# Optimization experiments

Hardware: AMD Instinct MI355X
Metric: run time of the kernel (lower is better)

The kernel has to match this reference:

```python
import jax, jax.numpy as jnp
import numpy as np

N_R, N_S, D, L = 20000, 5000, 512, 3

def setup_inputs() -> dict:
    key = jax.random.key(0)
    ks = jax.random.split(key, 7)
    s = 1.0 / np.sqrt(D)  # xavier-ish scale to keep activations bounded
    return {
        "h_s": jax.random.normal(ks[0], (N_S, D), jnp.float32),
        "A_rs": jax.random.uniform(ks[1], (N_R, N_S), jnp.float32),
        "r_embed": jax.random.normal(ks[2], (N_R, D), jnp.float32) * s,
        "Wr": jax.random.normal(ks[3], (L, D, D), jnp.float32) * s,  # reading self-transform per layer
        "Ws": jax.random.normal(ks[4], (L, D, D), jnp.float32) * s,  # skill->reading cross-transform
        "Vr": jax.random.normal(ks[5], (L, D, D), jnp.float32) * s,  # reading->skill cross-transform
        "Vs": jax.random.normal(ks[6], (L, D, D), jnp.float32) * s,  # skill self-transform
    }

def reference(h_s, A_rs, r_embed, Wr, Ws, Vr, Vs):
    # ReadingGCNStage.forward: h = dropout(r_embed.weight) (eval-mode no-op),
    # then BipartiteGCNStack(h_s, h, A_rs): per-layer degree-normalized bipartite
    # message passing with dense per-side transforms and ReLU.
    eps = 1e-6
    deg_r = A_rs.sum(axis=1, keepdims=True) + eps   # [N_R, 1] reading degrees
    deg_s = A_rs.sum(axis=0)[:, None] + eps          # [N_S, 1] skill degrees
    h_r = r_embed
    for l in range(Wr.shape[0]):  # fixed small n_layers
        m_r = (A_rs @ h_s) / deg_r        # [N_R, D] mean-aggregated skill msgs
        m_s = (A_rs.T @ h_r) / deg_s      # [N_S, D] mean-aggregated reading msgs
        h_r_new = jax.nn.relu(m_r @ Ws[l] + h_r @ Wr[l])
        h_s = jax.nn.relu(m_s @ Vr[l] + h_s @ Vs[l])
        h_r = h_r_new
    return h_r  # updated reading embeddings [N_R, D]
```

## Files before the change

### kernel.cpp

```cpp
#include <hip/hip_runtime.h>


typedef __bf16 bf16_t;
typedef __attribute__((ext_vector_type(8))) __bf16 bf16x8;
typedef __attribute__((ext_vector_type(4))) __bf16 bf16x4;
typedef __attribute__((ext_vector_type(4))) float f32x4;

#define N_R 20000
#define N_S 5000
#define DD  512
#define MR_PAD 20096
#define MS_PAD 5120
#define KS_PAD 5056
#define KR_PAD 20224

__device__ __forceinline__ void gll16(const bf16_t* g, bf16_t* l) {
  __builtin_amdgcn_global_load_lds(
      (const __attribute__((address_space(1))) void*)g,
      (__attribute__((address_space(3))) void*)l, 16, 0, 0);
}


__global__ __launch_bounds__(256) void conv_rowsum_A(
    const float* __restrict__ A, bf16_t* __restrict__ Ab, float* __restrict__ deg_r) {
  int r = blockIdx.x;
  int t = threadIdx.x;
  __shared__ float wsum[4];
  if (r < N_R) {
    const float4* Arow = (const float4*)(A + (size_t)r * N_S);
    float s = 0.f;
    for (int c4 = t; c4 < N_S / 4; c4 += 256) {
      float4 v = Arow[c4];
      s += v.x + v.y + v.z + v.w;
      bf16x4 pv;
      pv[0] = (bf16_t)v.x; pv[1] = (bf16_t)v.y; pv[2] = (bf16_t)v.z; pv[3] = (bf16_t)v.w;
      *(bf16x4*)(Ab + (size_t)r * KS_PAD + 4 * c4) = pv;
    }
    if (t < KS_PAD - N_S) Ab[(size_t)r * KS_PAD + N_S + t] = (bf16_t)0.f;
    for (int off = 32; off > 0; off >>= 1) s += __shfl_down(s, off, 64);
    if ((t & 63) == 0) wsum[t >> 6] = s;
    __syncthreads();
    if (t == 0) deg_r[r] = wsum[0] + wsum[1] + wsum[2] + wsum[3] + 1e-6f;
  } else {
    for (int c = t; c < KS_PAD; c += 256) Ab[(size_t)r * KS_PAD + c] = (bf16_t)0.f;
  }
}

__global__ void init_deg_s(float* __restrict__ deg_s) {
  int i = blockIdx.x * 256 + threadIdx.x;
  if (i < N_S) deg_s[i] = 1e-6f;
}

__global__ __launch_bounds__(256) void transpose_A_deg(
    const bf16_t* __restrict__ Ab, bf16_t* __restrict__ At, float* __restrict__ deg_s) {
  __shared__ float tile[64][65];
  __shared__ float csum[4][64];
  int rt = blockIdx.x * 64;
  int st = blockIdx.y * 64;
  int tx = threadIdx.x & 63;
  int ty = threadIdx.x >> 6;
  int s = st + tx;
  float part = 0.f;
  for (int i = 0; i < 16; ++i) {
    int rr = ty * 16 + i;
    int r = rt + rr;
    float v = 0.f;
    if (r < N_R && s < KS_PAD) v = (float)Ab[(size_t)r * KS_PAD + s];
    tile[rr][tx] = v;
    part += v;
  }
  csum[ty][tx] = part;
  __syncthreads();
  if (ty == 0 && s < N_S)
    atomicAdd(&deg_s[s], csum[0][tx] + csum[1][tx] + csum[2][tx] + csum[3][tx]);
  for (int i = 0; i < 16; ++i) {
    int rr = ty * 16 + i;
    int r = rt + tx;
    if (r < KR_PAD) At[(size_t)(st + rr) * KR_PAD + r] = (bf16_t)tile[tx][rr];
  }
}

template <typename SrcT>
__global__ __launch_bounds__(256) void transpose_to_bf16(
    const SrcT* __restrict__ src, int R, int C, bf16_t* __restrict__ dst, int ldd) {
  __shared__ float tile[64][65];
  int rt = blockIdx.x * 64;
  int ct = blockIdx.y * 64;
  int tx = threadIdx.x & 63;
  int ty = threadIdx.x >> 6;
  for (int i = 0; i < 16; ++i) {
    int rr = ty * 16 + i;
    int r = rt + rr;
    float v = 0.f;
    if (r < R) v = (float)src[(size_t)r * C + ct + tx];
    tile[rr][tx] = v;
  }
  __syncthreads();
  for (int i = 0; i < 16; ++i) {
    int rr = ty * 16 + i;
    int r = rt + tx;
    if (r < ldd) dst[(size_t)(ct + rr) * ldd + r] = (bf16_t)tile[tx][rr];
  }
}

__global__ __launch_bounds__(256) void transpose_weights(
    const float* __restrict__ Wr, const float* __restrict__ Ws,
    const float* __restrict__ Vr, const float* __restrict__ Vs,
    bf16_t* __restrict__ WT) {
  int z = blockIdx.z;
  int t4 = z & 3, l = z >> 2;
  const float* srcs[4] = {Wr, Ws, Vr, Vs};
  const float* src = srcs[t4] + (size_t)l * DD * DD;
  bf16_t* dst = WT + (size_t)z * DD * DD;
  __shared__ float tile[64][65];
  int rt = blockIdx.x * 64, ct = blockIdx.y * 64;
  int tx = threadIdx.x & 63, ty = threadIdx.x >> 6;
  for (int i = 0; i < 16; ++i) {
    int rr = ty * 16 + i;
    tile[rr][tx] = src[(size_t)(rt + rr) * DD + ct + tx];
  }
  __syncthreads();
  for (int i = 0; i < 16; ++i) {
    int rr = ty * 16 + i;
    dst[(size_t)(ct + rr) * DD + rt + tx] = (bf16_t)tile[tx][rr];
  }
}

__global__ __launch_bounds__(256) void conv_pad(
    const float* __restrict__ src, bf16_t* __restrict__ dst, int R, int Rp) {
  size_t i = (size_t)blockIdx.x * 256 + threadIdx.x;
  size_t tot = (size_t)Rp * DD;
  if (i < tot) {
    int r = (int)(i / DD);
    dst[i] = (r < R) ? (bf16_t)src[i] : (bf16_t)0.f;
  }
}

__global__ __launch_bounds__(256) void combine_div(
    const float* __restrict__ part, int S, size_t stride,
    const float* __restrict__ deg, int Mreal, int Mpad, bf16_t* __restrict__ out) {
  size_t base = ((size_t)blockIdx.x * 256 + threadIdx.x) * 4;
  if (base >= (size_t)Mpad * DD) return;
  f32x4 s = *(const f32x4*)(part + base);
  for (int k = 1; k < S; ++k) s += *(const f32x4*)(part + (size_t)k * stride + base);
  int r = (int)(base >> 9);
  float inv = (r < Mreal) ? 1.0f / deg[r] : 0.f;
  bf16x4 o;
  o[0] = (bf16_t)(s[0] * inv); o[1] = (bf16_t)(s[1] * inv);
  o[2] = (bf16_t)(s[2] * inv); o[3] = (bf16_t)(s[3] * inv);
  *(bf16x4*)(out + base) = o;
}

template <bool HAS2, int EPI>
__global__ __launch_bounds__(256) void gemm64(
    const bf16_t* __restrict__ A1, const bf16_t* __restrict__ B1, int kt1, int lda1, int ldb1,
    const bf16_t* __restrict__ A2, const bf16_t* __restrict__ B2, int kt2, int lda2, int ldb2,
    int kt_chunk,
    bf16_t* __restrict__ Cb, int Mreal, const float* __restrict__ deg,
    float* __restrict__ Cf, float* __restrict__ Cpart, size_t part_stride) {
  __shared__ bf16_t As[2 * 128 * 32];
  __shared__ bf16_t Bs[2 * 128 * 32];
  const int tid = threadIdx.x;
  const int lane = tid & 63;
  const int wave = tid >> 6;
  const int m0 = blockIdx.x * 128;
  const int n0 = blockIdx.y * 128;
  const int lrow = lane >> 2;
  const int lcol = (lane & 3) * 8;
  const int wm = (wave >> 1) * 64;
  const int wn = (wave & 1) * 64;
  const int lr = lane & 15;
  const int quad = lane >> 4;

  f32x4 acc[4][4] = {};

  const int ktot = kt1 + (HAS2 ? kt2 : 0);
  const int ktb = blockIdx.z * kt_chunk;
  const int kte = (ktb + kt_chunk < ktot) ? ktb + kt_chunk : ktot;

  for (int kt = ktb; kt < kte; ++kt) {
    const bf16_t* Ap; const bf16_t* Bp; int lda, ldb, k0;
    if (!HAS2 || kt < kt1) { Ap = A1; Bp = B1; lda = lda1; ldb = ldb1; k0 = kt * 64; }
    else                   { Ap = A2; Bp = B2; lda = lda2; ldb = ldb2; k0 = (kt - kt1) * 64; }
#pragma unroll
    for (int g = 0; g < 4; ++g) {
      const int h = g >> 1;
      const int rb = (g & 1) * 64 + wave * 16;
      gll16(Ap + (size_t)(m0 + rb + lrow) * lda + k0 + h * 32 + lcol,
            &As[h * 4096 + rb * 32]);
      gll16(Bp + (size_t)(n0 + rb + lrow) * ldb + k0 + h * 32 + lcol,
            &Bs[h * 4096 + rb * 32]);
    }
    __syncthreads();
    bf16x8 af[2][4], bq[2][4];
#pragma unroll
    for (int h = 0; h < 2; ++h)
#pragma unroll
      for (int i = 0; i < 4; ++i) {
        af[h][i] = *(const bf16x8*)&As[h * 4096 + (wm + i * 16 + lr) * 32 + quad * 8];
        bq[h][i] = *(const bf16x8*)&Bs[h * 4096 + (wn + i * 16 + lr) * 32 + quad * 8];
      }
#pragma unroll
    for (int h = 0; h < 2; ++h)
#pragma unroll
      for (int i = 0; i < 4; ++i)
#pragma unroll
        for (int j = 0; j < 4; ++j)
          acc[i][j] = __builtin_amdgcn_mfma_f32_16x16x32_bf16(af[h][i], bq[h][j], acc[i][j], 0, 0, 0);
    __syncthreads();
  }

  if (EPI == 2) {
    float* P = Cpart + blockIdx.z * part_stride;
#pragma unroll
    for (int i = 0; i < 4; ++i)
#pragma unroll
      for (int j = 0; j < 4; ++j) {
        int c = n0 + wn + j * 16 + lr;
#pragma unroll
        for (int g = 0; g < 4; ++g) {
          int r = m0 + wm + i * 16 + quad * 4 + g;
          P[(size_t)r * DD + c] = acc[i][j][g];
        }
      }
  } else {
#pragma unroll
    for (int i = 0; i < 4; ++i)
#pragma unroll
      for (int j = 0; j < 4; ++j) {
        int c = n0 + wn + j * 16 + lr;
#pragma unroll
        for (int g = 0; g < 4; ++g) {
          int r = m0 + wm + i * 16 + quad * 4 + g;
          if (r < Mreal) {
            float v = acc[i][j][g];
            if (EPI == 0) v /= deg[r];
            else v = fmaxf(v, 0.f);
            Cb[(size_t)r * DD + c] = (bf16_t)v;
            if (EPI == 1 && Cf != nullptr) Cf[(size_t)r * DD + c] = v;
          }
        }
      }
  }
}

extern "C" void kernel_launch(void* const* d_in, const int* in_sizes, int n_in,
                              void* d_out, int out_size, void* d_ws, size_t ws_size,
                              hipStream_t stream) {
  const float* h_s0 = (const float*)d_in[0];
  const float* A    = (const float*)d_in[1];
  const float* r_em = (const float*)d_in[2];
  const float* Wr   = (const float*)d_in[3];
  const float* Ws   = (const float*)d_in[4];
  const float* Vr   = (const float*)d_in[5];
  const float* Vs   = (const float*)d_in[6];
  float* out = (float*)d_out;

  char* p = (char*)d_ws;
  auto alloc = [&](size_t bytes) {
    char* q = p;
    p += (bytes + 255) & ~(size_t)255;
    return q;
  };
  bf16_t* Ab  = (bf16_t*)alloc((size_t)MR_PAD * KS_PAD * 2);
  bf16_t* At  = (bf16_t*)alloc((size_t)MS_PAD * KR_PAD * 2);
  bf16_t* hsT = (bf16_t*)alloc((size_t)DD * KS_PAD * 2);
  bf16_t* hrT = (bf16_t*)alloc((size_t)DD * KR_PAD * 2);
  bf16_t* WT  = (bf16_t*)alloc((size_t)12 * DD * DD * 2);
  bf16_t* hs_b[2] = {(bf16_t*)alloc((size_t)MS_PAD * DD * 2), (bf16_t*)alloc((size_t)MS_PAD * DD * 2)};
  bf16_t* hr_b[2] = {(bf16_t*)alloc((size_t)MR_PAD * DD * 2), (bf16_t*)alloc((size_t)MR_PAD * DD * 2)};
  bf16_t* mr_b = (bf16_t*)alloc((size_t)MR_PAD * DD * 2);
  bf16_t* ms_b = (bf16_t*)alloc((size_t)MS_PAD * DD * 2);
  float* deg_r = (float*)alloc((size_t)N_R * 4);
  float* deg_s = (float*)alloc((size_t)N_S * 4);
  size_t core_bytes = (size_t)(p - (char*)d_ws);
  size_t part_stride_r = (size_t)MR_PAD * DD;
  size_t part_stride_s = (size_t)MS_PAD * DD;
  size_t part_bytes = (part_stride_s * 8 > part_stride_r * 2 ? part_stride_s * 8 : part_stride_r * 2) * 4;
  bool split_ok = (core_bytes + part_bytes + 256 <= ws_size);
  float* part = split_ok ? (float*)alloc(part_bytes) : nullptr;
  if (core_bytes > ws_size) return;

  conv_rowsum_A<<<MR_PAD, 256, 0, stream>>>(A, Ab, deg_r);
  init_deg_s<<<(N_S + 255) / 256, 256, 0, stream>>>(deg_s);
  transpose_A_deg<<<dim3(316, 80), 256, 0, stream>>>(Ab, At, deg_s);
  transpose_to_bf16<float><<<dim3(79, 8), 256, 0, stream>>>(h_s0, N_S, DD, hsT, KS_PAD);
  transpose_to_bf16<float><<<dim3(316, 8), 256, 0, stream>>>(r_em, N_R, DD, hrT, KR_PAD);
  transpose_weights<<<dim3(8, 8, 12), 256, 0, stream>>>(Wr, Ws, Vr, Vs, WT);
  conv_pad<<<(MS_PAD * DD) / 256, 256, 0, stream>>>(h_s0, hs_b[0], N_S, MS_PAD);
  conv_pad<<<(MR_PAD * DD) / 256, 256, 0, stream>>>(r_em, hr_b[0], N_R, MR_PAD);

  const int ktA = KS_PAD / 64;
  const int ktT = KR_PAD / 64;

  int cur = 0;
  for (int l = 0; l < 3; ++l) {
    bf16_t* WrT = WT + ((size_t)l * 4 + 0) * DD * DD;
    bf16_t* WsT = WT + ((size_t)l * 4 + 1) * DD * DD;
    bf16_t* VrT = WT + ((size_t)l * 4 + 2) * DD * DD;
    bf16_t* VsT = WT + ((size_t)l * 4 + 3) * DD * DD;

    if (split_ok) {
      gemm64<false, 2><<<dim3(157, 4, 2), 256, 0, stream>>>(
          Ab, hsT, ktA, KS_PAD, KS_PAD, nullptr, nullptr, 0, 0, 0,
          40, nullptr, N_R, nullptr, nullptr, part, part_stride_r);
      combine_div<<<MR_PAD / 2, 256, 0, stream>>>(part, 2, part_stride_r, deg_r, N_R, MR_PAD, mr_b);
    } else {
      gemm64<false, 0><<<dim3(157, 4, 1), 256, 0, stream>>>(
          Ab, hsT, ktA, KS_PAD, KS_PAD, nullptr, nullptr, 0, 0, 0,
          ktA, mr_b, N_R, deg_r, nullptr, nullptr, 0);
    }
    if (l < 2) {
      if (split_ok) {
        gemm64<false, 2><<<dim3(40, 4, 8), 256, 0, stream>>>(
            At, hrT, ktT, KR_PAD, KR_PAD, nullptr, nullptr, 0, 0, 0,
            40, nullptr, N_S, nullptr, nullptr, part, part_stride_s);
        combine_div<<<MS_PAD / 2, 256, 0, stream>>>(part, 8, part_stride_s, deg_s, N_S, MS_PAD, ms_b);
      } else {
        gemm64<false, 0><<<dim3(40, 4, 1), 256, 0, stream>>>(
            At, hrT, ktT, KR_PAD, KR_PAD, nullptr, nullptr, 0, 0, 0,
            ktT, ms_b, N_S, deg_s, nullptr, nullptr, 0);
      }
    }
    gemm64<true, 1><<<dim3(157, 4, 1), 256, 0, stream>>>(
        mr_b, WsT, 8, DD, DD, hr_b[cur], WrT, 8, DD, DD,
        16, hr_b[1 - cur], N_R, nullptr, (l == 2) ? out : nullptr, nullptr, 0);
    if (l < 2) {
      gemm64<true, 1><<<dim3(40, 4, 1), 256, 0, stream>>>(
          ms_b, VrT, 8, DD, DD, hs_b[cur], VsT, 8, DD, DD,
          16, hs_b[1 - cur], N_S, nullptr, nullptr, nullptr, 0);
      transpose_to_bf16<bf16_t><<<dim3(316, 8), 256, 0, stream>>>(hr_b[1 - cur], N_R, DD, hrT, KR_PAD);
      transpose_to_bf16<bf16_t><<<dim3(79, 8), 256, 0, stream>>>(hs_b[1 - cur], N_S, DD, hsT, KS_PAD);
    }
    cur = 1 - cur;
  }
}
```

Measured before the change: 2.060 ms.

## Add 256x256-tile split-K GEMM with swizzled LDS for adjacency aggregations

Adds a new 512-thread GEMM kernel with 256x256 output tiles, 64-wide K steps, XOR-swizzled LDS, direct global-to-LDS loads and a four-phase double-buffered schedule with MFMA priority boosting. It replaces the 128x128 gemm64 for the two large adjacency aggregations (A@h_s and A^T@h_r), and changes the split-K factors to 3 and 6. The reading-side padding is raised to a multiple of 256 to suit the new tile. The larger tiles are meant to raise data reuse and MFMA density in the dominant GEMMs. The cost is higher register and LDS pressure, larger fp32 partial buffers and more combine traffic.

```diff
diff --git a/kernel.cpp b/kernel.cpp
--- a/kernel.cpp
+++ b/kernel.cpp
@@ -9,7 +9,7 @@
 #define N_R 20000
 #define N_S 5000
 #define DD  512
-#define MR_PAD 20096
+#define MR_PAD 20224
 #define MS_PAD 5120
 #define KS_PAD 5056
 #define KR_PAD 20224
@@ -149,6 +149,112 @@
   o[0] = (bf16_t)(s[0] * inv); o[1] = (bf16_t)(s[1] * inv);
   o[2] = (bf16_t)(s[2] * inv); o[3] = (bf16_t)(s[3] * inv);
   *(bf16x4*)(out + base) = o;
+}
+
+__global__ __launch_bounds__(512, 2) void gemm256(
+    const bf16_t* __restrict__ A, const bf16_t* __restrict__ B, int ld,
+    int kt_total, int kt_chunk, float* __restrict__ Cpart, size_t part_stride) {
+  __shared__ bf16_t As[2][256 * 64];
+  __shared__ bf16_t Bs[2][256 * 64];
+  const int tid = threadIdx.x;
+  const int lane = tid & 63;
+  const int wave = tid >> 6;
+  const int bid = blockIdx.x;
+  const int m0 = (bid >> 1) * 256;
+  const int n0 = (bid & 1) * 256;
+  const int z = blockIdx.y;
+  const int ktb = z * kt_chunk;
+  int kte = ktb + kt_chunk;
+  if (kte > kt_total) kte = kt_total;
+  if (ktb >= kte) return;
+  const int wm = (wave >> 2) * 128;
+  const int wn = (wave & 3) * 64;
+  const int lr = lane & 15;
+  const int quad = lane >> 4;
+  const int rloc = lane >> 3;
+  const int cel = ((lane & 7) ^ rloc) * 8;
+
+  auto SA = [&](int b, int q, int t) {
+    int k0 = (t < kte ? t : kte - 1) * 64;
+    gll16(A + (size_t)(m0 + q * 64 + wave * 8 + rloc) * ld + k0 + cel,
+          &As[b][(q * 64 + wave * 8) * 64]);
+  };
+  auto SB = [&](int b, int q, int t) {
+    int k0 = (t < kte ? t : kte - 1) * 64;
+    gll16(B + (size_t)(n0 + q * 64 + wave * 8 + rloc) * ld + k0 + cel,
+          &Bs[b][(q * 64 + wave * 8) * 64]);
+  };
+
+  f32x4 acc[8][4] = {};
+  bf16x8 af[4], bf[4];
+
+#define PHASE(BUF, MH, KS, READB, ...)                                           \
+  {                                                                              \
+    _Pragma("unroll")                                                            \
+    for (int i = 0; i < 4; ++i) {                                                \
+      int r = wm + (MH) * 64 + i * 16 + lr;                                      \
+      af[i] = *(const bf16x8*)&As[BUF][r * 64 +                                  \
+                                       (((KS) * 32 + quad * 8) ^ ((r & 7) * 8))];\
+    }                                                                            \
+    if (READB) {                                                                 \
+      _Pragma("unroll")                                                          \
+      for (int j = 0; j < 4; ++j) {                                              \
+        int r = wn + j * 16 + lr;                                                \
+        bf[j] = *(const bf16x8*)&Bs[BUF][r * 64 +                                \
+                                       (((KS) * 32 + quad * 8) ^ ((r & 7) * 8))];\
+      }                                                                          \
+    }                                                                            \
+    __VA_ARGS__;                                                                 \
+    __builtin_amdgcn_s_barrier();                                                \
+    asm volatile("s_waitcnt lgkmcnt(0)" ::: "memory");                           \
+    __builtin_amdgcn_s_setprio(1);                                               \
+    _Pragma("unroll")                                                            \
+    for (int i = 0; i < 4; ++i)                                                  \
+      _Pragma("unroll")                                                          \
+      for (int j = 0; j < 4; ++j)                                                \
+        acc[(MH) * 4 + i][j] = __builtin_amdgcn_mfma_f32_16x16x32_bf16(          \
+            af[i], bf[j], acc[(MH) * 4 + i][j], 0, 0, 0);                        \
+    __builtin_amdgcn_s_setprio(0);                                               \
+  }
+
+  SB(0, 0, ktb); SB(0, 1, ktb); SB(0, 2, ktb); SB(0, 3, ktb);
+  SA(0, 0, ktb); SA(0, 2, ktb);
+  SA(0, 1, ktb); SA(0, 3, ktb);
+  SB(1, 0, ktb + 1); SB(1, 1, ktb + 1);
+  asm volatile("s_waitcnt vmcnt(4)" ::: "memory");
+  __builtin_amdgcn_s_barrier();
+
+  const int nt = kte - ktb;
+  for (int ti = 0; ti < nt; ++ti) {
+    const int t = ktb + ti;
+    const int buf = ti & 1;
+    const int nb = buf ^ 1;
+    PHASE(buf, 0, 0, 1, SB(nb, 2, t + 1); SB(nb, 3, t + 1));
+    asm volatile("s_waitcnt vmcnt(4)" ::: "memory");
+    __builtin_amdgcn_s_barrier();
+    PHASE(buf, 1, 0, 0, SA(nb, 0, t + 1); SA(nb, 2, t + 1));
+    __builtin_amdgcn_s_barrier();
+    PHASE(buf, 0, 1, 1, SA(nb, 1, t + 1); SA(nb, 3, t + 1));
+    __builtin_amdgcn_s_barrier();
+    PHASE(buf, 1, 1, 0, SB(buf, 0, t + 2); SB(buf, 1, t + 2));
+    asm volatile("s_waitcnt vmcnt(4)" ::: "memory");
+    __builtin_amdgcn_s_barrier();
+  }
+  asm volatile("s_waitcnt vmcnt(0)" ::: "memory");
+#undef PHASE
+
+  float* P = Cpart + (size_t)z * part_stride;
+#pragma unroll
+  for (int ii = 0; ii < 8; ++ii)
+#pragma unroll
+    for (int j = 0; j < 4; ++j) {
+      int c = n0 + wn + j * 16 + lr;
+#pragma unroll
+      for (int g = 0; g < 4; ++g) {
+        int r = m0 + wm + ii * 16 + quad * 4 + g;
+        P[(size_t)r * DD + c] = acc[ii][j][g];
+      }
+    }
 }
 
 template <bool HAS2, int EPI>
@@ -276,7 +382,7 @@
   size_t core_bytes = (size_t)(p - (char*)d_ws);
   size_t part_stride_r = (size_t)MR_PAD * DD;
   size_t part_stride_s = (size_t)MS_PAD * DD;
-  size_t part_bytes = (part_stride_s * 8 > part_stride_r * 2 ? part_stride_s * 8 : part_stride_r * 2) * 4;
+  size_t part_bytes = (part_stride_r * 3 > part_stride_s * 6 ? part_stride_r * 3 : part_stride_s * 6) * 4;
   bool split_ok = (core_bytes + part_bytes + 256 <= ws_size);
   float* part = split_ok ? (float*)alloc(part_bytes) : nullptr;
   if (core_bytes > ws_size) return;
@@ -301,28 +407,28 @@
     bf16_t* VsT = WT + ((size_t)l * 4 + 3) * DD * DD;
 
     if (split_ok) {
-      gemm64<false, 2><<<dim3(157, 4, 2), 256, 0, stream>>>(
-          Ab, hsT, ktA, KS_PAD, KS_PAD, nullptr, nullptr, 0, 0, 0,
-          40, nullptr, N_R, nullptr, nullptr, part, part_stride_r);
-      combine_div<<<MR_PAD / 2, 256, 0, stream>>>(part, 2, part_stride_r, deg_r, N_R, MR_PAD, mr_b);
+      gemm256<<<dim3(79 * 2, 3), 512, 0, stream>>>(
+          Ab, hsT, KS_PAD, ktA, 27, part, part_stride_r);
+      combine_div<<<MR_PAD * DD / 1024, 256, 0, stream>>>(
+          part, 3, part_stride_r, deg_r, N_R, MR_PAD, mr_b);
     } else {
-      gemm64<false, 0><<<dim3(157, 4, 1), 256, 0, stream>>>(
+      gemm64<false, 0><<<dim3(158, 4, 1), 256, 0, stream>>>(
           Ab, hsT, ktA, KS_PAD, KS_PAD, nullptr, nullptr, 0, 0, 0,
           ktA, mr_b, N_R, deg_r, nullptr, nullptr, 0);
     }
     if (l < 2) {
       if (split_ok) {
-        gemm64<false, 2><<<dim3(40, 4, 8), 256, 0, stream>>>(
-            At, hrT, ktT, KR_PAD, KR_PAD, nullptr, nullptr, 0, 0, 0,
-            40, nullptr, N_S, nullptr, nullptr, part, part_stride_s);
-        combine_div<<<MS_PAD / 2, 256, 0, stream>>>(part, 8, part_stride_s, deg_s, N_S, MS_PAD, ms_b);
+        gemm256<<<dim3(20 * 2, 6), 512, 0, stream>>>(
+            At, hrT, KR_PAD, ktT, 53, part, part_stride_s);
+        combine_div<<<MS_PAD * DD / 1024, 256, 0, stream>>>(
+            part, 6, part_stride_s, deg_s, N_S, MS_PAD, ms_b);
       } else {
         gemm64<false, 0><<<dim3(40, 4, 1), 256, 0, stream>>>(
             At, hrT, ktT, KR_PAD, KR_PAD, nullptr, nullptr, 0, 0, 0,
             ktT, ms_b, N_S, deg_s, nullptr, nullptr, 0);
       }
     }
-    gemm64<true, 1><<<dim3(157, 4, 1), 256, 0, stream>>>(
+    gemm64<true, 1><<<dim3(158, 4, 1), 256, 0, stream>>>(
         mr_b, WsT, 8, DD, DD, hr_b[cur], WrT, 8, DD, DD,
         16, hr_b[1 - cur], N_R, nullptr, (l == 2) ? out : nullptr, nullptr, 0);
     if (l < 2) {
```

New measurement: 1.868 ms. -9.4%, faster.
